# Optimization experiments

Hardware: AMD Instinct MI355X
Metric: run time of the kernel (lower is better)

## Reference

```python
import jax, jax.numpy as jnp
import numpy as np

LSCALE = 0.001  # RBF lengthscale on /360-normalized coordinates (from convDeepSet(0.001, ...))
EPS = 1e-8


def setup_inputs() -> dict:
    key = jax.random.key(0)
    k1, k2, k3 = jax.random.split(key, 3)
    B, C, N, G1, G2 = 2, 26, 2048, 240, 121
    # station coordinates, /360-normalized as in the source (lon in [0,1], lat in [-0.25,0.25])
    x_lon = jax.random.uniform(k1, (B, N), dtype=jnp.float32)
    x_lat = jax.random.uniform(k2, (B, N), dtype=jnp.float32, minval=-0.25, maxval=0.25)
    wt = jax.random.normal(k3, (B, C, N), dtype=jnp.float32)
    # fixed internal grid from the source: linspace(0,360,240)/360 and linspace(-90,90,121)/360
    grid_lon = (jnp.linspace(0.0, 360.0, G1) / 360.0).astype(jnp.float32)
    grid_lat = (jnp.linspace(-90.0, 90.0, G2) / 360.0).astype(jnp.float32)
    return {"x_lon": x_lon, "x_lat": x_lat, "wt": wt, "grid_lon": grid_lon, "grid_lat": grid_lat}


def reference(x_lon, x_lat, wt, grid_lon, grid_lat):
    """Batched OffToOn RBF SetConv with density channel (fused over C channels).

    x_lon, x_lat: [B, N] scattered station coords
    wt:           [B, C, N] observed values (NaN = missing)
    grid_lon:     [G1], grid_lat: [G2]
    returns [B, 2C, G1, G2]: density-normalized data channels then density channels.
    """
    inv2l2 = 0.5 / (LSCALE * LSCALE)
    # separable RBF kernel weights station -> grid
    kx = jnp.exp(-inv2l2 * (x_lon[:, :, None] - grid_lon[None, None, :]) ** 2)  # [B,N,G1]
    ky = jnp.exp(-inv2l2 * (x_lat[:, :, None] - grid_lat[None, None, :]) ** 2)  # [B,N,G2]
    finite = jnp.isfinite(wt)
    mask = finite.astype(wt.dtype)          # [B,C,N] density weights (missing -> 0)
    w = jnp.where(finite, wt, 0.0)          # [B,C,N] masked values
    # weighted scatter onto grid: sum_n w[b,c,n] * kx[b,n,g] * ky[b,n,h]
    data = jnp.einsum('bcn,bng,bnh->bcgh', w, kx, ky)        # [B,C,G1,G2]
    density = jnp.einsum('bcn,bng,bnh->bcgh', mask, kx, ky)  # [B,C,G1,G2]
    data_norm = data / jnp.maximum(density, EPS)
    return jnp.concatenate([data_norm, density], axis=1)  # [B,2C,G1,G2]
```

## Files before the change

kernel.cpp:

```cpp
#include <hip/hip_runtime.h>
#include <math.h>

#define BB 2
#define CC 26
#define NN 2048
#define G1 240
#define G2 121
#define INV2L2 5.0e5f
#define EPSV 1e-8f
#define CUT 42.0f
#define HSPLIT 2
#define HTILE 61
#define MCAPT 192
#define BCAP 16
#define WTS 193

__global__ __launch_bounds__(256) void setconv_binned(
    const float* __restrict__ x_lon,
    const float* __restrict__ x_lat,
    const float* __restrict__ wt,
    const float* __restrict__ grid_lon,
    const float* __restrict__ grid_lat,
    float* __restrict__ out)
{
    __shared__ float s_wt[CC][WTS];
    __shared__ float s_ax[MCAPT];
    __shared__ float s_lat[MCAPT];
    __shared__ int   s_n[MCAPT];
    __shared__ int   s_hlo[MCAPT];
    __shared__ float s_bw[HTILE][BCAP + 1];
    __shared__ int   s_bi[HTILE][BCAP + 1];
    __shared__ int   s_cnt[HTILE];
    __shared__ float s_glat[G2];
    __shared__ int   s_count;

    const int tid = threadIdx.x;
    const int blk = blockIdx.x;
    const int ht  = blk % HSPLIT;
    const int bg  = blk / HSPLIT;
    const int b   = bg / G1;
    const int g   = bg % G1;
    const int t0   = ht * HTILE;
    const int tend = min(G2, t0 + HTILE);
    const int th   = tend - t0;

    if (tid == 0) s_count = 0;
    if (tid < HTILE) s_cnt[tid] = 0;
    if (tid < G2) s_glat[tid] = grid_lat[tid];
    __syncthreads();

    const float glon  = grid_lon[g];
    const float glat0 = s_glat[0];
    const float inv_dlat = (float)(G2 - 1) / (s_glat[G2 - 1] - glat0);

    const int n0 = tid * 8;
    float lon[8], lat[8];
    {
        const float4* pl = (const float4*)&x_lon[b * NN + n0];
        const float4* pa = (const float4*)&x_lat[b * NN + n0];
        const float4 l0 = pl[0], l1 = pl[1];
        const float4 a0 = pa[0], a1 = pa[1];
        lon[0]=l0.x; lon[1]=l0.y; lon[2]=l0.z; lon[3]=l0.w;
        lon[4]=l1.x; lon[5]=l1.y; lon[6]=l1.z; lon[7]=l1.w;
        lat[0]=a0.x; lat[1]=a0.y; lat[2]=a0.z; lat[3]=a0.w;
        lat[4]=a1.x; lat[5]=a1.y; lat[6]=a1.z; lat[7]=a1.w;
    }
    float axv[8];
    int   hlov[8];
    unsigned mask = 0;
    int hits = 0;
    #pragma unroll
    for (int k = 0; k < 8; ++k) {
        const float dx = lon[k] - glon;
        axv[k] = dx * dx * INV2L2;
        const float hc = (lat[k] - glat0) * inv_dlat;
        hlov[k] = max(0, (int)ceilf(hc) - 3);
        if (axv[k] <= CUT && hlov[k] <= tend - 1 && hlov[k] + 7 >= t0) {
            mask |= 1u << k; ++hits;
        }
    }
    int pos = 0;
    if (hits) pos = atomicAdd(&s_count, hits);
    #pragma unroll
    for (int k = 0; k < 8; ++k) {
        if ((mask & (1u << k)) && pos < MCAPT) {
            s_n[pos]   = n0 + k;
            s_ax[pos]  = axv[k];
            s_lat[pos] = lat[k];
            s_hlo[pos] = hlov[k];
            ++pos;
        }
    }
    __syncthreads();
    const int M = min(s_count, MCAPT);

    for (int base = 0; base < M; base += 64) {
        for (int v = tid; v < CC * 64; v += 256) {
            const int i = base + (v & 63);
            const int c = v >> 6;
            if (i < M) s_wt[c][i] = wt[(b * CC + c) * NN + s_n[i]];
        }
    }
    for (int v = tid; v < M * 8; v += 256) {
        const int i = v >> 3;
        const int j = v & 7;
        const int h = s_hlo[i] + j;
        if (h >= t0 && h < tend) {
            const float dy = s_lat[i] - s_glat[h];
            const float a  = s_ax[i] + dy * dy * INV2L2;
            if (a <= CUT) {
                const int e = atomicAdd(&s_cnt[h - t0], 1);
                if (e < BCAP) {
                    s_bw[h - t0][e] = __expf(-a);
                    s_bi[h - t0][e] = i;
                }
            }
        }
    }
    __syncthreads();

    const int hh = tid >> 2;
    const int q  = tid & 3;
    const int co = (q == 0) ? 0 : (q == 1) ? 7 : (q == 2) ? 13 : 20;
    const int cn = (q & 1) ? 6 : 7;

    if (hh < th) {
        const int h = t0 + hh;
        float accd[7], accm[7];
        #pragma unroll
        for (int k = 0; k < 7; ++k) { accd[k] = 0.f; accm[k] = 0.f; }

        const int cnt = min(s_cnt[hh], BCAP);
        for (int e = 0; e < cnt; ++e) {
            const float s = s_bw[hh][e];
            const int   i = s_bi[hh][e];
            #pragma unroll
            for (int k = 0; k < 7; ++k) {
                if (k < cn) {
                    const float raw = s_wt[co + k][i];
                    const unsigned ex = (__float_as_uint(raw) >> 23) & 255u;
                    const bool fin = (ex != 255u);
                    accd[k] += s * (fin ? raw : 0.f);
                    accm[k] += s * (fin ? 1.f : 0.f);
                }
            }
        }
        #pragma unroll
        for (int k = 0; k < 7; ++k) {
            if (k < cn) {
                const int c = co + k;
                const size_t o1 = (((size_t)b * 2 * CC + c)      * G1 + g) * G2 + h;
                const size_t o2 = (((size_t)b * 2 * CC + CC + c) * G1 + g) * G2 + h;
                out[o1] = accd[k] / fmaxf(accm[k], EPSV);
                out[o2] = accm[k];
            }
        }
    }
}

extern "C" void kernel_launch(void* const* d_in, const int* in_sizes, int n_in,
                              void* d_out, int out_size, void* d_ws, size_t ws_size,
                              hipStream_t stream) {
    const float* x_lon    = (const float*)d_in[0];
    const float* x_lat    = (const float*)d_in[1];
    const float* wt       = (const float*)d_in[2];
    const float* grid_lon = (const float*)d_in[3];
    const float* grid_lat = (const float*)d_in[4];
    float* out = (float*)d_out;

    dim3 grid(BB * G1 * HSPLIT);
    dim3 block(256);
    setconv_binned<<<grid, block, 0, stream>>>(x_lon, x_lat, wt, grid_lon, grid_lat, out);
}
```

Before: 14.28 us.

## Drop shared-memory station compaction; bin stations directly and read weights from global

Removes the two-pass station compaction and the shared-memory staging of wt values. Each thread now bins its own stations straight into per-latitude buckets, storing the station index, and the accumulation loop reads wt directly from global memory (likely L2/L1 hits). This cuts barriers, about 20KB of LDS and the gather pass. In exchange the inner loop does scattered global loads, and each thread runs a variable-length inner loop over latitude rows.

```diff
diff --git a/kernel.cpp b/kernel.cpp
--- a/kernel.cpp
+++ b/kernel.cpp
@@ -11,11 +11,10 @@
 #define CUT 42.0f
 #define HSPLIT 2
 #define HTILE 61
-#define MCAPT 192
 #define BCAP 16
-#define WTS 193
+#define BSTR 17
 
-__global__ __launch_bounds__(256) void setconv_binned(
+__global__ __launch_bounds__(256) void setconv_direct(
     const float* __restrict__ x_lon,
     const float* __restrict__ x_lat,
     const float* __restrict__ wt,
@@ -23,16 +22,10 @@
     const float* __restrict__ grid_lat,
     float* __restrict__ out)
 {
-    __shared__ float s_wt[CC][WTS];
-    __shared__ float s_ax[MCAPT];
-    __shared__ float s_lat[MCAPT];
-    __shared__ int   s_n[MCAPT];
-    __shared__ int   s_hlo[MCAPT];
-    __shared__ float s_bw[HTILE][BCAP + 1];
-    __shared__ int   s_bi[HTILE][BCAP + 1];
+    __shared__ float s_bw[HTILE][BSTR];
+    __shared__ int   s_bn[HTILE][BSTR];
     __shared__ int   s_cnt[HTILE];
     __shared__ float s_glat[G2];
-    __shared__ int   s_count;
 
     const int tid = threadIdx.x;
     const int blk = blockIdx.x;
@@ -43,15 +36,6 @@
     const int t0   = ht * HTILE;
     const int tend = min(G2, t0 + HTILE);
     const int th   = tend - t0;
-
-    if (tid == 0) s_count = 0;
-    if (tid < HTILE) s_cnt[tid] = 0;
-    if (tid < G2) s_glat[tid] = grid_lat[tid];
-    __syncthreads();
-
-    const float glon  = grid_lon[g];
-    const float glat0 = s_glat[0];
-    const float inv_dlat = (float)(G2 - 1) / (s_glat[G2 - 1] - glat0);
 
     const int n0 = tid * 8;
     float lon[8], lat[8];
@@ -65,54 +49,33 @@
         lat[0]=a0.x; lat[1]=a0.y; lat[2]=a0.z; lat[3]=a0.w;
         lat[4]=a1.x; lat[5]=a1.y; lat[6]=a1.z; lat[7]=a1.w;
     }
-    float axv[8];
-    int   hlov[8];
-    unsigned mask = 0;
-    int hits = 0;
+
+    if (tid < HTILE) s_cnt[tid] = 0;
+    if (tid < G2) s_glat[tid] = grid_lat[tid];
+    __syncthreads();
+
+    const float glon  = grid_lon[g];
+    const float glat0 = s_glat[0];
+    const float inv_dlat = (float)(G2 - 1) / (s_glat[G2 - 1] - glat0);
+
     #pragma unroll
     for (int k = 0; k < 8; ++k) {
         const float dx = lon[k] - glon;
-        axv[k] = dx * dx * INV2L2;
-        const float hc = (lat[k] - glat0) * inv_dlat;
-        hlov[k] = max(0, (int)ceilf(hc) - 3);
-        if (axv[k] <= CUT && hlov[k] <= tend - 1 && hlov[k] + 7 >= t0) {
-            mask |= 1u << k; ++hits;
-        }
-    }
-    int pos = 0;
-    if (hits) pos = atomicAdd(&s_count, hits);
-    #pragma unroll
-    for (int k = 0; k < 8; ++k) {
-        if ((mask & (1u << k)) && pos < MCAPT) {
-            s_n[pos]   = n0 + k;
-            s_ax[pos]  = axv[k];
-            s_lat[pos] = lat[k];
-            s_hlo[pos] = hlov[k];
-            ++pos;
-        }
-    }
-    __syncthreads();
-    const int M = min(s_count, MCAPT);
-
-    for (int base = 0; base < M; base += 64) {
-        for (int v = tid; v < CC * 64; v += 256) {
-            const int i = base + (v & 63);
-            const int c = v >> 6;
-            if (i < M) s_wt[c][i] = wt[(b * CC + c) * NN + s_n[i]];
-        }
-    }
-    for (int v = tid; v < M * 8; v += 256) {
-        const int i = v >> 3;
-        const int j = v & 7;
-        const int h = s_hlo[i] + j;
-        if (h >= t0 && h < tend) {
-            const float dy = s_lat[i] - s_glat[h];
-            const float a  = s_ax[i] + dy * dy * INV2L2;
-            if (a <= CUT) {
-                const int e = atomicAdd(&s_cnt[h - t0], 1);
-                if (e < BCAP) {
-                    s_bw[h - t0][e] = __expf(-a);
-                    s_bi[h - t0][e] = i;
+        const float ax = dx * dx * INV2L2;
+        if (ax <= CUT) {
+            const float hc  = (lat[k] - glat0) * inv_dlat;
+            const int   hlo = max(0, (int)ceilf(hc) - 3);
+            const int jlo = max(t0, hlo);
+            const int jhi = min(tend - 1, hlo + 7);
+            for (int h = jlo; h <= jhi; ++h) {
+                const float dy = lat[k] - s_glat[h];
+                const float a  = ax + dy * dy * INV2L2;
+                if (a <= CUT) {
+                    const int e = atomicAdd(&s_cnt[h - t0], 1);
+                    if (e < BCAP) {
+                        s_bw[h - t0][e] = __expf(-a);
+                        s_bn[h - t0][e] = n0 + k;
+                    }
                 }
             }
         }
@@ -133,11 +96,12 @@
         const int cnt = min(s_cnt[hh], BCAP);
         for (int e = 0; e < cnt; ++e) {
             const float s = s_bw[hh][e];
-            const int   i = s_bi[hh][e];
+            const int   n = s_bn[hh][e];
+            const float* wp = &wt[((size_t)b * CC + co) * NN + n];
             #pragma unroll
             for (int k = 0; k < 7; ++k) {
                 if (k < cn) {
-                    const float raw = s_wt[co + k][i];
+                    const float raw = wp[(size_t)k * NN];
                     const unsigned ex = (__float_as_uint(raw) >> 23) & 255u;
                     const bool fin = (ex != 255u);
                     accd[k] += s * (fin ? raw : 0.f);
@@ -170,5 +134,5 @@
 
     dim3 grid(BB * G1 * HSPLIT);
     dim3 block(256);
-    setconv_binned<<<grid, block, 0, stream>>>(x_lon, x_lat, wt, grid_lon, grid_lat, out);
+    setconv_direct<<<grid, block, 0, stream>>>(x_lon, x_lat, wt, grid_lon, grid_lat, out);
 }
```

Result: slower. 19.23 us (+34.7%).

## Process full latitude column per block with 512 threads instead of splitting

Applied to the files above, without the earlier changes.

Drops the two-way latitude split so each block covers a whole grid-longitude column (all 121 latitudes) using 512 threads. Each station is filtered, gathered and binned once per column rather than once per half, removing duplicate wt gathers and duplicate kernel-weight computation. The trade is half as many blocks (480), each with more shared memory and threads, which lowers the number of independent blocks available to spread across the GPU.

```diff
diff --git a/kernel.cpp b/kernel.cpp
--- a/kernel.cpp
+++ b/kernel.cpp
@@ -9,13 +9,13 @@
 #define INV2L2 5.0e5f
 #define EPSV 1e-8f
 #define CUT 42.0f
-#define HSPLIT 2
-#define HTILE 61
 #define MCAPT 192
 #define BCAP 16
 #define WTS 193
+#define BSTR 17
 
-__global__ __launch_bounds__(256) void setconv_binned(
+
+__global__ __launch_bounds__(512) void setconv_col512(
     const float* __restrict__ x_lon,
     const float* __restrict__ x_lat,
     const float* __restrict__ wt,
@@ -28,61 +28,49 @@
     __shared__ float s_lat[MCAPT];
     __shared__ int   s_n[MCAPT];
     __shared__ int   s_hlo[MCAPT];
-    __shared__ float s_bw[HTILE][BCAP + 1];
-    __shared__ int   s_bi[HTILE][BCAP + 1];
-    __shared__ int   s_cnt[HTILE];
+    __shared__ float s_bw[G2][BSTR];
+    __shared__ int   s_bi[G2][BSTR];
+    __shared__ int   s_cnt[G2];
     __shared__ float s_glat[G2];
     __shared__ int   s_count;
 
     const int tid = threadIdx.x;
-    const int blk = blockIdx.x;
-    const int ht  = blk % HSPLIT;
-    const int bg  = blk / HSPLIT;
-    const int b   = bg / G1;
-    const int g   = bg % G1;
-    const int t0   = ht * HTILE;
-    const int tend = min(G2, t0 + HTILE);
-    const int th   = tend - t0;
+    const int b   = blockIdx.x / G1;
+    const int g   = blockIdx.x % G1;
+
+    const int n0 = tid * 4;
+    float lon[4], lat[4];
+    {
+        const float4 l0 = *(const float4*)&x_lon[b * NN + n0];
+        const float4 a0 = *(const float4*)&x_lat[b * NN + n0];
+        lon[0]=l0.x; lon[1]=l0.y; lon[2]=l0.z; lon[3]=l0.w;
+        lat[0]=a0.x; lat[1]=a0.y; lat[2]=a0.z; lat[3]=a0.w;
+    }
 
     if (tid == 0) s_count = 0;
-    if (tid < HTILE) s_cnt[tid] = 0;
-    if (tid < G2) s_glat[tid] = grid_lat[tid];
+    if (tid < G2) { s_cnt[tid] = 0; s_glat[tid] = grid_lat[tid]; }
     __syncthreads();
 
     const float glon  = grid_lon[g];
     const float glat0 = s_glat[0];
     const float inv_dlat = (float)(G2 - 1) / (s_glat[G2 - 1] - glat0);
 
-    const int n0 = tid * 8;
-    float lon[8], lat[8];
-    {
-        const float4* pl = (const float4*)&x_lon[b * NN + n0];
-        const float4* pa = (const float4*)&x_lat[b * NN + n0];
-        const float4 l0 = pl[0], l1 = pl[1];
-        const float4 a0 = pa[0], a1 = pa[1];
-        lon[0]=l0.x; lon[1]=l0.y; lon[2]=l0.z; lon[3]=l0.w;
-        lon[4]=l1.x; lon[5]=l1.y; lon[6]=l1.z; lon[7]=l1.w;
-        lat[0]=a0.x; lat[1]=a0.y; lat[2]=a0.z; lat[3]=a0.w;
-        lat[4]=a1.x; lat[5]=a1.y; lat[6]=a1.z; lat[7]=a1.w;
-    }
-    float axv[8];
-    int   hlov[8];
+    float axv[4];
+    int   hlov[4];
     unsigned mask = 0;
     int hits = 0;
     #pragma unroll
-    for (int k = 0; k < 8; ++k) {
+    for (int k = 0; k < 4; ++k) {
         const float dx = lon[k] - glon;
         axv[k] = dx * dx * INV2L2;
         const float hc = (lat[k] - glat0) * inv_dlat;
         hlov[k] = max(0, (int)ceilf(hc) - 3);
-        if (axv[k] <= CUT && hlov[k] <= tend - 1 && hlov[k] + 7 >= t0) {
-            mask |= 1u << k; ++hits;
-        }
+        if (axv[k] <= CUT) { mask |= 1u << k; ++hits; }
     }
     int pos = 0;
     if (hits) pos = atomicAdd(&s_count, hits);
     #pragma unroll
-    for (int k = 0; k < 8; ++k) {
+    for (int k = 0; k < 4; ++k) {
         if ((mask & (1u << k)) && pos < MCAPT) {
             s_n[pos]   = n0 + k;
             s_ax[pos]  = axv[k];
@@ -95,24 +83,24 @@
     const int M = min(s_count, MCAPT);
 
     for (int base = 0; base < M; base += 64) {
-        for (int v = tid; v < CC * 64; v += 256) {
+        for (int v = tid; v < CC * 64; v += 512) {
             const int i = base + (v & 63);
             const int c = v >> 6;
             if (i < M) s_wt[c][i] = wt[(b * CC + c) * NN + s_n[i]];
         }
     }
-    for (int v = tid; v < M * 8; v += 256) {
+    for (int v = tid; v < M * 8; v += 512) {
         const int i = v >> 3;
         const int j = v & 7;
         const int h = s_hlo[i] + j;
-        if (h >= t0 && h < tend) {
+        if (h < G2) {
             const float dy = s_lat[i] - s_glat[h];
             const float a  = s_ax[i] + dy * dy * INV2L2;
             if (a <= CUT) {
-                const int e = atomicAdd(&s_cnt[h - t0], 1);
+                const int e = atomicAdd(&s_cnt[h], 1);
                 if (e < BCAP) {
-                    s_bw[h - t0][e] = __expf(-a);
-                    s_bi[h - t0][e] = i;
+                    s_bw[h][e] = __expf(-a);
+                    s_bi[h][e] = i;
                 }
             }
         }
@@ -124,8 +112,7 @@
     const int co = (q == 0) ? 0 : (q == 1) ? 7 : (q == 2) ? 13 : 20;
     const int cn = (q & 1) ? 6 : 7;
 
-    if (hh < th) {
-        const int h = t0 + hh;
+    if (hh < G2) {
         float accd[7], accm[7];
         #pragma unroll
         for (int k = 0; k < 7; ++k) { accd[k] = 0.f; accm[k] = 0.f; }
@@ -149,8 +136,8 @@
         for (int k = 0; k < 7; ++k) {
             if (k < cn) {
                 const int c = co + k;
-                const size_t o1 = (((size_t)b * 2 * CC + c)      * G1 + g) * G2 + h;
-                const size_t o2 = (((size_t)b * 2 * CC + CC + c) * G1 + g) * G2 + h;
+                const size_t o1 = (((size_t)b * 2 * CC + c)      * G1 + g) * G2 + hh;
+                const size_t o2 = (((size_t)b * 2 * CC + CC + c) * G1 + g) * G2 + hh;
                 out[o1] = accd[k] / fmaxf(accm[k], EPSV);
                 out[o2] = accm[k];
             }
@@ -168,7 +155,7 @@
     const float* grid_lat = (const float*)d_in[4];
     float* out = (float*)d_out;
 
-    dim3 grid(BB * G1 * HSPLIT);
-    dim3 block(256);
-    setconv_binned<<<grid, block, 0, stream>>>(x_lon, x_lat, wt, grid_lon, grid_lat, out);
+    dim3 grid(BB * G1);
+    dim3 block(512);
+    setconv_col512<<<grid, block, 0, stream>>>(x_lon, x_lat, wt, grid_lon, grid_lat, out);
 }
```

New measurement: 13.61 us. -4.7%, faster.
